# Optimization experiments

Hardware: AMD Instinct MI355X
Metric: run time of the kernel (lower is better)

## Reference

```python
import jax, jax.numpy as jnp
import numpy as np

N_NODES = 200000
D_FEAT = 128
B = 40000
DEG = 16
E = B * DEG
D_OUT = 256
N_CLASSES = 128


def setup_inputs() -> dict:
    key = jax.random.key(0)
    ks = jax.random.split(key, 8)
    inputs = jax.random.randint(ks[0], (B,), 0, N_NODES)
    neighbor_ids = jax.random.randint(ks[1], (E,), 0, N_NODES)
    segment_ids = jnp.repeat(jnp.arange(B, dtype=jnp.int64 if jax.config.jax_enable_x64 else jnp.int32), DEG)
    feat_data = jax.random.normal(ks[2], (N_NODES, D_FEAT), dtype=jnp.float32)
    W1 = jax.random.normal(ks[3], (D_OUT, 2 * D_FEAT), dtype=jnp.float32) * 0.05
    b1 = jax.random.normal(ks[4], (D_OUT,), dtype=jnp.float32) * 0.05
    W3 = jax.random.normal(ks[5], (N_CLASSES, D_OUT), dtype=jnp.float32) * 0.05
    b3 = jax.random.normal(ks[6], (N_CLASSES,), dtype=jnp.float32) * 0.05
    return {"inputs": inputs, "neighbor_ids": neighbor_ids, "segment_ids": segment_ids,
            "feat_data": feat_data, "W1": W1, "b1": b1, "W3": W3, "b3": b3}


def reference(inputs, neighbor_ids, segment_ids, feat_data, W1, b1, W3, b3):
    # Segment-mean over neighbor features (replaces Python per-node loop)
    neigh = feat_data[neighbor_ids]                               # [E, D]
    sums = jax.ops.segment_sum(neigh, segment_ids, num_segments=B)  # [B, D]
    cnt = jax.ops.segment_sum(jnp.ones((E,), jnp.float32), segment_ids, num_segments=B)
    means = sums / jnp.maximum(cnt, 1.0)[:, None]                 # [B, D]
    # Concat self + neighbor-mean, linear1
    emb = jnp.concatenate([feat_data[inputs], means], axis=1)     # [B, 2D]
    h = emb @ W1.T + b1                                           # [B, D_OUT]
    # ReLU -> linear3 -> L2 normalize (F.normalize, eps=1e-12)
    logits = jax.nn.relu(h) @ W3.T + b3                           # [B, n_classes]
    norm = jnp.linalg.norm(logits, axis=1, keepdims=True)
    return logits / jnp.maximum(norm, 1e-12)
```

## Files before the change

### kernel.cpp

```cpp
#include <hip/hip_runtime.h>
#include <stdint.h>

#define NNODES 200000
#define BNODES 40000
#define DEG    16
#define DFEAT  128
#define DOUT   256
#define NCLS   128
#define TILE   16

typedef __attribute__((ext_vector_type(8))) __bf16 bf16x8;
typedef __attribute__((ext_vector_type(4))) float  floatx4;

__device__ __forceinline__ uint32_t f2bf(float f) {
  uint32_t x = __float_as_uint(f);
  return ((x + 0x7fffu + ((x >> 16) & 1u)) >> 16) & 0xffffu;
}
__device__ __forceinline__ float bf2f(uint16_t u) {
  return __uint_as_float((uint32_t)u << 16);
}

__global__ __launch_bounds__(256) void cvt_weights(
    const float* __restrict__ W1, const float* __restrict__ W3,
    uint16_t* __restrict__ w1b, uint16_t* __restrict__ w3b) {
  int i = blockIdx.x * 256 + threadIdx.x;
  if (i < DOUT * 2 * DFEAT) w1b[i] = (uint16_t)f2bf(W1[i]);
  if (i < NCLS * DOUT)      w3b[i] = (uint16_t)f2bf(W3[i]);
}

__global__ __launch_bounds__(256) void cvt_feat(
    const float* __restrict__ feat, uint16_t* __restrict__ featb) {
  const size_t i = ((size_t)blockIdx.x * 256 + threadIdx.x) * 16;
  const float4 f0 = *(const float4*)(feat + i + 0);
  const float4 f1 = *(const float4*)(feat + i + 4);
  const float4 f2 = *(const float4*)(feat + i + 8);
  const float4 f3 = *(const float4*)(feat + i + 12);
  uint4 p0, p1;
  p0.x = f2bf(f0.x) | (f2bf(f0.y) << 16);
  p0.y = f2bf(f0.z) | (f2bf(f0.w) << 16);
  p0.z = f2bf(f1.x) | (f2bf(f1.y) << 16);
  p0.w = f2bf(f1.z) | (f2bf(f1.w) << 16);
  p1.x = f2bf(f2.x) | (f2bf(f2.y) << 16);
  p1.y = f2bf(f2.z) | (f2bf(f2.w) << 16);
  p1.z = f2bf(f3.x) | (f2bf(f3.y) << 16);
  p1.w = f2bf(f3.z) | (f2bf(f3.w) << 16);
  *(uint4*)(featb + i)     = p0;
  *(uint4*)(featb + i + 8) = p1;
}

template <bool BF16T>
__global__ __launch_bounds__(256, 8) void sage_fused(
    const int* __restrict__ inputs, const int* __restrict__ nbr,
    const float* __restrict__ feat, const uint16_t* __restrict__ featb,
    const uint16_t* __restrict__ w1b, const float* __restrict__ b1,
    const uint16_t* __restrict__ w3b, const float* __restrict__ b3,
    float* __restrict__ out) {
  __shared__ __align__(16) unsigned char smemA[TILE * 264 * 2];
  __shared__ __align__(16) uint16_t hL[TILE][264];
  uint16_t (*embL)[264] = (uint16_t (*)[264])smemA;
  float    (*lgL)[132]  = (float    (*)[132])smemA;

  const int tid  = threadIdx.x;
  const int w    = __builtin_amdgcn_readfirstlane(tid >> 6);
  const int lane = tid & 63;
  const int quad = lane >> 4;
  const int l16  = lane & 15;

  {
    const int nodeBase = blockIdx.x * TILE + w * 4;
    if constexpr (BF16T) {
      const uint16_t* fb = featb + lane * 2;
#pragma unroll
      for (int p = 0; p < 4; p += 2) {
        const int nA = nodeBase + p, nB = nodeBase + p + 1;
        const int* nbA = nbr + nA * DEG;
        const int* nbB = nbr + nB * DEG;
        const int sA = inputs[nA], sB = inputs[nB];
        ushort2 rA[16], rB[16];
#pragma unroll
        for (int j = 0; j < 16; ++j)
          rA[j] = *(const ushort2*)(fb + (size_t)nbA[j] * DFEAT);
        const ushort2 svA = *(const ushort2*)(fb + (size_t)sA * DFEAT);
#pragma unroll
        for (int j = 0; j < 16; ++j)
          rB[j] = *(const ushort2*)(fb + (size_t)nbB[j] * DFEAT);
        const ushort2 svB = *(const ushort2*)(fb + (size_t)sB * DFEAT);
        {
          const float sx = (((bf2f(rA[0].x) + bf2f(rA[1].x)) + (bf2f(rA[2].x) + bf2f(rA[3].x)))
                          + ((bf2f(rA[4].x) + bf2f(rA[5].x)) + (bf2f(rA[6].x) + bf2f(rA[7].x))))
                         + (((bf2f(rA[8].x) + bf2f(rA[9].x)) + (bf2f(rA[10].x) + bf2f(rA[11].x)))
                          + ((bf2f(rA[12].x) + bf2f(rA[13].x)) + (bf2f(rA[14].x) + bf2f(rA[15].x))));
          const float sy = (((bf2f(rA[0].y) + bf2f(rA[1].y)) + (bf2f(rA[2].y) + bf2f(rA[3].y)))
                          + ((bf2f(rA[4].y) + bf2f(rA[5].y)) + (bf2f(rA[6].y) + bf2f(rA[7].y))))
                         + (((bf2f(rA[8].y) + bf2f(rA[9].y)) + (bf2f(rA[10].y) + bf2f(rA[11].y)))
                          + ((bf2f(rA[12].y) + bf2f(rA[13].y)) + (bf2f(rA[14].y) + bf2f(rA[15].y))));
          const int row = w * 4 + p;
          *(uint32_t*)&embL[row][lane * 2]         = (uint32_t)svA.x | ((uint32_t)svA.y << 16);
          *(uint32_t*)&embL[row][DFEAT + lane * 2] = f2bf(sx * 0.0625f) | (f2bf(sy * 0.0625f) << 16);
        }
        {
          const float sx = (((bf2f(rB[0].x) + bf2f(rB[1].x)) + (bf2f(rB[2].x) + bf2f(rB[3].x)))
                          + ((bf2f(rB[4].x) + bf2f(rB[5].x)) + (bf2f(rB[6].x) + bf2f(rB[7].x))))
                         + (((bf2f(rB[8].x) + bf2f(rB[9].x)) + (bf2f(rB[10].x) + bf2f(rB[11].x)))
                          + ((bf2f(rB[12].x) + bf2f(rB[13].x)) + (bf2f(rB[14].x) + bf2f(rB[15].x))));
          const float sy = (((bf2f(rB[0].y) + bf2f(rB[1].y)) + (bf2f(rB[2].y) + bf2f(rB[3].y)))
                          + ((bf2f(rB[4].y) + bf2f(rB[5].y)) + (bf2f(rB[6].y) + bf2f(rB[7].y))))
                         + (((bf2f(rB[8].y) + bf2f(rB[9].y)) + (bf2f(rB[10].y) + bf2f(rB[11].y)))
                          + ((bf2f(rB[12].y) + bf2f(rB[13].y)) + (bf2f(rB[14].y) + bf2f(rB[15].y))));
          const int row = w * 4 + p + 1;
          *(uint32_t*)&embL[row][lane * 2]         = (uint32_t)svB.x | ((uint32_t)svB.y << 16);
          *(uint32_t*)&embL[row][DFEAT + lane * 2] = f2bf(sx * 0.0625f) | (f2bf(sy * 0.0625f) << 16);
        }
      }
    } else {
      const float* fb = feat + lane * 2;
#pragma unroll
      for (int p = 0; p < 4; ++p) {
        const int node = nodeBase + p;
        const int* nb  = nbr + node * DEG;
        const int self = inputs[node];
        float2 r[16];
#pragma unroll
        for (int j = 0; j < 16; ++j)
          r[j] = *(const float2*)(fb + (size_t)nb[j] * DFEAT);
        const float2 sv = *(const float2*)(fb + (size_t)self * DFEAT);
        const float sx = (((r[0].x + r[1].x) + (r[2].x + r[3].x)) + ((r[4].x + r[5].x) + (r[6].x + r[7].x)))
                       + (((r[8].x + r[9].x) + (r[10].x + r[11].x)) + ((r[12].x + r[13].x) + (r[14].x + r[15].x)));
        const float sy = (((r[0].y + r[1].y) + (r[2].y + r[3].y)) + ((r[4].y + r[5].y) + (r[6].y + r[7].y)))
                       + (((r[8].y + r[9].y) + (r[10].y + r[11].y)) + ((r[12].y + r[13].y) + (r[14].y + r[15].y)));
        const int row = w * 4 + p;
        *(uint32_t*)&embL[row][lane * 2]         = f2bf(sv.x) | (f2bf(sv.y) << 16);
        *(uint32_t*)&embL[row][DFEAT + lane * 2] = f2bf(sx * 0.0625f) | (f2bf(sy * 0.0625f) << 16);
      }
    }
  }
  __syncthreads();

  const int kq = quad * 8;

  {
    floatx4 acc[4];
#pragma unroll
    for (int ot = 0; ot < 4; ++ot) {
      floatx4 z = {0.f, 0.f, 0.f, 0.f};
      acc[ot] = z;
    }
#pragma unroll
    for (int kt = 0; kt < 8; ++kt) {
      const int k0 = kt * 32 + kq;
      const bf16x8 a = *(const bf16x8*)&embL[l16][k0];
#pragma unroll
      for (int ot = 0; ot < 4; ++ot) {
        const int o = w * 64 + ot * 16 + l16;
        const bf16x8 b = *(const bf16x8*)(w1b + o * 256 + k0);
        acc[ot] = __builtin_amdgcn_mfma_f32_16x16x32_bf16(a, b, acc[ot], 0, 0, 0);
      }
    }
#pragma unroll
    for (int ot = 0; ot < 4; ++ot) {
      const int o = w * 64 + ot * 16 + l16;
      const float bias = b1[o];
#pragma unroll
      for (int r = 0; r < 4; ++r) {
        float v = acc[ot][r] + bias;
        v = fmaxf(v, 0.f);
        hL[quad * 4 + r][o] = (uint16_t)f2bf(v);
      }
    }
  }
  __syncthreads();

  {
    floatx4 acc2[2];
#pragma unroll
    for (int ct = 0; ct < 2; ++ct) {
      floatx4 z = {0.f, 0.f, 0.f, 0.f};
      acc2[ct] = z;
    }
#pragma unroll
    for (int kt = 0; kt < 8; ++kt) {
      const int k0 = kt * 32 + kq;
      const bf16x8 a = *(const bf16x8*)&hL[l16][k0];
#pragma unroll
      for (int ct = 0; ct < 2; ++ct) {
        const int c = w * 32 + ct * 16 + l16;
        const bf16x8 b = *(const bf16x8*)(w3b + c * 256 + k0);
        acc2[ct] = __builtin_amdgcn_mfma_f32_16x16x32_bf16(a, b, acc2[ct], 0, 0, 0);
      }
    }
#pragma unroll
    for (int ct = 0; ct < 2; ++ct) {
      const int c = w * 32 + ct * 16 + l16;
      const float bias = b3[c];
#pragma unroll
      for (int r = 0; r < 4; ++r)
        lgL[quad * 4 + r][c] = acc2[ct][r] + bias;
    }
  }
  __syncthreads();

  {
    const int nr  = tid >> 4;
    const int sub = tid & 15;
    const float* lrow = &lgL[nr][sub * 8];
    float4 v0 = *(const float4*)(lrow + 0);
    float4 v1 = *(const float4*)(lrow + 4);
    float ss = v0.x * v0.x + v0.y * v0.y + v0.z * v0.z + v0.w * v0.w
             + v1.x * v1.x + v1.y * v1.y + v1.z * v1.z + v1.w * v1.w;
    ss += __shfl_xor(ss, 1);
    ss += __shfl_xor(ss, 2);
    ss += __shfl_xor(ss, 4);
    ss += __shfl_xor(ss, 8);
    const float scale = 1.f / fmaxf(sqrtf(ss), 1e-12f);
    v0.x *= scale; v0.y *= scale; v0.z *= scale; v0.w *= scale;
    v1.x *= scale; v1.y *= scale; v1.z *= scale; v1.w *= scale;
    float* op = out + ((size_t)(blockIdx.x * TILE + nr)) * NCLS + sub * 8;
    *(float4*)(op + 0) = v0;
    *(float4*)(op + 4) = v1;
  }
}

extern "C" void kernel_launch(void* const* d_in, const int* in_sizes, int n_in,
                              void* d_out, int out_size, void* d_ws, size_t ws_size,
                              hipStream_t stream) {
  const int*   inputs = (const int*)d_in[0];
  const int*   nbr    = (const int*)d_in[1];
  const float* feat   = (const float*)d_in[3];
  const float* W1     = (const float*)d_in[4];
  const float* b1     = (const float*)d_in[5];
  const float* W3     = (const float*)d_in[6];
  const float* b3     = (const float*)d_in[7];

  uint16_t* w1b   = (uint16_t*)d_ws;
  uint16_t* w3b   = w1b + DOUT * 2 * DFEAT;
  uint16_t* featb = w3b + NCLS * DOUT;

  const size_t need = ((size_t)(DOUT * 2 * DFEAT + NCLS * DOUT)
                     + (size_t)NNODES * DFEAT) * sizeof(uint16_t);

  cvt_weights<<<(DOUT * 2 * DFEAT) / 256, 256, 0, stream>>>(W1, W3, w1b, w3b);
  if (ws_size >= need) {
    cvt_feat<<<(NNODES * DFEAT) / (256 * 16), 256, 0, stream>>>(feat, featb);
    sage_fused<true><<<BNODES / TILE, 256, 0, stream>>>(
        inputs, nbr, feat, featb, w1b, b1, w3b, b3, (float*)d_out);
  } else {
    sage_fused<false><<<BNODES / TILE, 256, 0, stream>>>(
        inputs, nbr, feat, nullptr, w1b, b1, w3b, b3, (float*)d_out);
  }
}
```

Before: 246.5 us.

## Store gathered neighbor features as FP8 and fuse conversion kernels

Converts the feature table to a custom FP8 (e4m3-like) encoding instead of bf16, halving the bytes written during conversion and read during the neighbor gather. The gather is restructured so each lane loads 8 bytes from one of four neighbors and partial sums are combined with cross-lane shuffles. Self features are now read directly from the fp32 table. The weight and feature conversion kernels are merged into one launch, and the occupancy hint drops from 8 to 6 waves. The cost is reduced precision of the neighbor mean, which risks accuracy tolerance.

```diff
diff --git a/kernel.cpp b/kernel.cpp
--- a/kernel.cpp
+++ b/kernel.cpp
@@ -9,6 +9,8 @@
 #define NCLS   128
 #define TILE   16
 
+#define FEAT_CVT_BLOCKS 6250
+
 typedef __attribute__((ext_vector_type(8))) __bf16 bf16x8;
 typedef __attribute__((ext_vector_type(4))) float  floatx4;
 
@@ -16,8 +18,23 @@
   uint32_t x = __float_as_uint(f);
   return ((x + 0x7fffu + ((x >> 16) & 1u)) >> 16) & 0xffffu;
 }
-__device__ __forceinline__ float bf2f(uint16_t u) {
-  return __uint_as_float((uint32_t)u << 16);
+
+__device__ __forceinline__ uint32_t f2fp8(float f) {
+  uint32_t u = __float_as_uint(f);
+  uint32_t s = (u >> 24) & 0x80u;
+  uint32_t a = u & 0x7fffffffu;
+  if (a >= 0x43E80000u) return s | 0x7Eu;
+  if (a < 0x3C800000u) {
+    uint32_t q = (uint32_t)rintf(__uint_as_float(a) * 512.0f);
+    return s | q;
+  }
+  uint32_t r = a + 0x7FFFFu + ((a >> 20) & 1u);
+  return s | ((r >> 20) - (120u << 3));
+}
+
+__device__ __forceinline__ float fp82f(uint32_t b) {
+  uint32_t x = ((b & 0x80u) << 24) | ((b & 0x7Fu) << 20);
+  return __uint_as_float(x) * __uint_as_float(0x7B800000u);
 }
 
 __global__ __launch_bounds__(256) void cvt_weights(
@@ -28,30 +45,34 @@
   if (i < NCLS * DOUT)      w3b[i] = (uint16_t)f2bf(W3[i]);
 }
 
-__global__ __launch_bounds__(256) void cvt_feat(
-    const float* __restrict__ feat, uint16_t* __restrict__ featb) {
-  const size_t i = ((size_t)blockIdx.x * 256 + threadIdx.x) * 16;
-  const float4 f0 = *(const float4*)(feat + i + 0);
-  const float4 f1 = *(const float4*)(feat + i + 4);
-  const float4 f2 = *(const float4*)(feat + i + 8);
-  const float4 f3 = *(const float4*)(feat + i + 12);
-  uint4 p0, p1;
-  p0.x = f2bf(f0.x) | (f2bf(f0.y) << 16);
-  p0.y = f2bf(f0.z) | (f2bf(f0.w) << 16);
-  p0.z = f2bf(f1.x) | (f2bf(f1.y) << 16);
-  p0.w = f2bf(f1.z) | (f2bf(f1.w) << 16);
-  p1.x = f2bf(f2.x) | (f2bf(f2.y) << 16);
-  p1.y = f2bf(f2.z) | (f2bf(f2.w) << 16);
-  p1.z = f2bf(f3.x) | (f2bf(f3.y) << 16);
-  p1.w = f2bf(f3.z) | (f2bf(f3.w) << 16);
-  *(uint4*)(featb + i)     = p0;
-  *(uint4*)(featb + i + 8) = p1;
-}
-
-template <bool BF16T>
-__global__ __launch_bounds__(256, 8) void sage_fused(
+__global__ __launch_bounds__(256) void cvt_all(
+    const float* __restrict__ feat, const float* __restrict__ W1,
+    const float* __restrict__ W3, uint8_t* __restrict__ featb8,
+    uint16_t* __restrict__ w1b, uint16_t* __restrict__ w3b) {
+  const int b = blockIdx.x;
+  if (b < FEAT_CVT_BLOCKS) {
+    const size_t i = ((size_t)b * 256 + threadIdx.x) * 16;
+    const float4 f0 = *(const float4*)(feat + i + 0);
+    const float4 f1 = *(const float4*)(feat + i + 4);
+    const float4 f2 = *(const float4*)(feat + i + 8);
+    const float4 f3 = *(const float4*)(feat + i + 12);
+    uint4 p;
+    p.x = f2fp8(f0.x) | (f2fp8(f0.y) << 8) | (f2fp8(f0.z) << 16) | (f2fp8(f0.w) << 24);
+    p.y = f2fp8(f1.x) | (f2fp8(f1.y) << 8) | (f2fp8(f1.z) << 16) | (f2fp8(f1.w) << 24);
+    p.z = f2fp8(f2.x) | (f2fp8(f2.y) << 8) | (f2fp8(f2.z) << 16) | (f2fp8(f2.w) << 24);
+    p.w = f2fp8(f3.x) | (f2fp8(f3.y) << 8) | (f2fp8(f3.z) << 16) | (f2fp8(f3.w) << 24);
+    *(uint4*)(featb8 + i) = p;
+  } else {
+    const int i = (b - FEAT_CVT_BLOCKS) * 256 + threadIdx.x;
+    if (i < DOUT * 2 * DFEAT) w1b[i] = (uint16_t)f2bf(W1[i]);
+    if (i < NCLS * DOUT)      w3b[i] = (uint16_t)f2bf(W3[i]);
+  }
+}
+
+template <bool FP8T>
+__global__ __launch_bounds__(256, 6) void sage_fused(
     const int* __restrict__ inputs, const int* __restrict__ nbr,
-    const float* __restrict__ feat, const uint16_t* __restrict__ featb,
+    const float* __restrict__ feat, const uint8_t* __restrict__ featb8,
     const uint16_t* __restrict__ w1b, const float* __restrict__ b1,
     const uint16_t* __restrict__ w3b, const float* __restrict__ b3,
     float* __restrict__ out) {
@@ -68,48 +89,63 @@
 
   {
     const int nodeBase = blockIdx.x * TILE + w * 4;
-    if constexpr (BF16T) {
-      const uint16_t* fb = featb + lane * 2;
+    if constexpr (FP8T) {
+      const uint8_t* fb = featb8 + (lane & 15) * 8;
 #pragma unroll
       for (int p = 0; p < 4; p += 2) {
         const int nA = nodeBase + p, nB = nodeBase + p + 1;
         const int* nbA = nbr + nA * DEG;
         const int* nbB = nbr + nB * DEG;
         const int sA = inputs[nA], sB = inputs[nB];
-        ushort2 rA[16], rB[16];
-#pragma unroll
-        for (int j = 0; j < 16; ++j)
-          rA[j] = *(const ushort2*)(fb + (size_t)nbA[j] * DFEAT);
-        const ushort2 svA = *(const ushort2*)(fb + (size_t)sA * DFEAT);
-#pragma unroll
-        for (int j = 0; j < 16; ++j)
-          rB[j] = *(const ushort2*)(fb + (size_t)nbB[j] * DFEAT);
-        const ushort2 svB = *(const ushort2*)(fb + (size_t)sB * DFEAT);
-        {
-          const float sx = (((bf2f(rA[0].x) + bf2f(rA[1].x)) + (bf2f(rA[2].x) + bf2f(rA[3].x)))
-                          + ((bf2f(rA[4].x) + bf2f(rA[5].x)) + (bf2f(rA[6].x) + bf2f(rA[7].x))))
-                         + (((bf2f(rA[8].x) + bf2f(rA[9].x)) + (bf2f(rA[10].x) + bf2f(rA[11].x)))
-                          + ((bf2f(rA[12].x) + bf2f(rA[13].x)) + (bf2f(rA[14].x) + bf2f(rA[15].x))));
-          const float sy = (((bf2f(rA[0].y) + bf2f(rA[1].y)) + (bf2f(rA[2].y) + bf2f(rA[3].y)))
-                          + ((bf2f(rA[4].y) + bf2f(rA[5].y)) + (bf2f(rA[6].y) + bf2f(rA[7].y))))
-                         + (((bf2f(rA[8].y) + bf2f(rA[9].y)) + (bf2f(rA[10].y) + bf2f(rA[11].y)))
-                          + ((bf2f(rA[12].y) + bf2f(rA[13].y)) + (bf2f(rA[14].y) + bf2f(rA[15].y))));
-          const int row = w * 4 + p;
-          *(uint32_t*)&embL[row][lane * 2]         = (uint32_t)svA.x | ((uint32_t)svA.y << 16);
-          *(uint32_t*)&embL[row][DFEAT + lane * 2] = f2bf(sx * 0.0625f) | (f2bf(sy * 0.0625f) << 16);
+        uint2 gA[4], gB[4];
+#pragma unroll
+        for (int k = 0; k < 4; ++k) {
+          const int i0 = nbA[4 * k + 0], i1 = nbA[4 * k + 1];
+          const int i2 = nbA[4 * k + 2], i3 = nbA[4 * k + 3];
+          const int lo  = (lane & 16) ? i1 : i0;
+          const int hi  = (lane & 16) ? i3 : i2;
+          const int rid = (lane & 32) ? hi : lo;
+          gA[k] = *(const uint2*)(fb + (size_t)rid * DFEAT);
         }
-        {
-          const float sx = (((bf2f(rB[0].x) + bf2f(rB[1].x)) + (bf2f(rB[2].x) + bf2f(rB[3].x)))
-                          + ((bf2f(rB[4].x) + bf2f(rB[5].x)) + (bf2f(rB[6].x) + bf2f(rB[7].x))))
-                         + (((bf2f(rB[8].x) + bf2f(rB[9].x)) + (bf2f(rB[10].x) + bf2f(rB[11].x)))
-                          + ((bf2f(rB[12].x) + bf2f(rB[13].x)) + (bf2f(rB[14].x) + bf2f(rB[15].x))));
-          const float sy = (((bf2f(rB[0].y) + bf2f(rB[1].y)) + (bf2f(rB[2].y) + bf2f(rB[3].y)))
-                          + ((bf2f(rB[4].y) + bf2f(rB[5].y)) + (bf2f(rB[6].y) + bf2f(rB[7].y))))
-                         + (((bf2f(rB[8].y) + bf2f(rB[9].y)) + (bf2f(rB[10].y) + bf2f(rB[11].y)))
-                          + ((bf2f(rB[12].y) + bf2f(rB[13].y)) + (bf2f(rB[14].y) + bf2f(rB[15].y))));
-          const int row = w * 4 + p + 1;
-          *(uint32_t*)&embL[row][lane * 2]         = (uint32_t)svB.x | ((uint32_t)svB.y << 16);
-          *(uint32_t*)&embL[row][DFEAT + lane * 2] = f2bf(sx * 0.0625f) | (f2bf(sy * 0.0625f) << 16);
+        const float2 svA = *(const float2*)(feat + (size_t)sA * DFEAT + lane * 2);
+#pragma unroll
+        for (int k = 0; k < 4; ++k) {
+          const int i0 = nbB[4 * k + 0], i1 = nbB[4 * k + 1];
+          const int i2 = nbB[4 * k + 2], i3 = nbB[4 * k + 3];
+          const int lo  = (lane & 16) ? i1 : i0;
+          const int hi  = (lane & 16) ? i3 : i2;
+          const int rid = (lane & 32) ? hi : lo;
+          gB[k] = *(const uint2*)(fb + (size_t)rid * DFEAT);
+        }
+        const float2 svB = *(const float2*)(feat + (size_t)sB * DFEAT + lane * 2);
+#pragma unroll
+        for (int nn = 0; nn < 2; ++nn) {
+          const uint2* g = nn ? gB : gA;
+          const float2 sv = nn ? svB : svA;
+          const int row = w * 4 + p + nn;
+          float acc[8] = {0.f, 0.f, 0.f, 0.f, 0.f, 0.f, 0.f, 0.f};
+#pragma unroll
+          for (int k = 0; k < 4; ++k) {
+            const uint32_t lo = g[k].x, hi = g[k].y;
+#pragma unroll
+            for (int j = 0; j < 4; ++j) {
+              acc[j]     += fp82f((lo >> (8 * j)) & 0xffu);
+              acc[4 + j] += fp82f((hi >> (8 * j)) & 0xffu);
+            }
+          }
+#pragma unroll
+          for (int j = 0; j < 8; ++j) {
+            acc[j] += __shfl_xor(acc[j], 16);
+            acc[j] += __shfl_xor(acc[j], 32);
+          }
+          uint4 mp;
+          mp.x = f2bf(acc[0] * 0.0625f) | (f2bf(acc[1] * 0.0625f) << 16);
+          mp.y = f2bf(acc[2] * 0.0625f) | (f2bf(acc[3] * 0.0625f) << 16);
+          mp.z = f2bf(acc[4] * 0.0625f) | (f2bf(acc[5] * 0.0625f) << 16);
+          mp.w = f2bf(acc[6] * 0.0625f) | (f2bf(acc[7] * 0.0625f) << 16);
+          *(uint32_t*)&embL[row][lane * 2] = f2bf(sv.x) | (f2bf(sv.y) << 16);
+          if (lane < 16)
+            *(uint4*)&embL[row][DFEAT + lane * 8] = mp;
         }
       }
     } else {
@@ -231,19 +267,20 @@
   const float* W3     = (const float*)d_in[6];
   const float* b3     = (const float*)d_in[7];
 
-  uint16_t* w1b   = (uint16_t*)d_ws;
-  uint16_t* w3b   = w1b + DOUT * 2 * DFEAT;
-  uint16_t* featb = w3b + NCLS * DOUT;
-
-  const size_t need = ((size_t)(DOUT * 2 * DFEAT + NCLS * DOUT)
-                     + (size_t)NNODES * DFEAT) * sizeof(uint16_t);
-
-  cvt_weights<<<(DOUT * 2 * DFEAT) / 256, 256, 0, stream>>>(W1, W3, w1b, w3b);
+  uint16_t* w1b    = (uint16_t*)d_ws;
+  uint16_t* w3b    = w1b + DOUT * 2 * DFEAT;
+  uint8_t*  featb8 = (uint8_t*)(w3b + NCLS * DOUT);
+
+  const size_t need = (size_t)(DOUT * 2 * DFEAT + NCLS * DOUT) * sizeof(uint16_t)
+                    + (size_t)NNODES * DFEAT;
+
   if (ws_size >= need) {
-    cvt_feat<<<(NNODES * DFEAT) / (256 * 16), 256, 0, stream>>>(feat, featb);
+    cvt_all<<<FEAT_CVT_BLOCKS + (DOUT * 2 * DFEAT) / 256, 256, 0, stream>>>(
+        feat, W1, W3, featb8, w1b, w3b);
     sage_fused<true><<<BNODES / TILE, 256, 0, stream>>>(
-        inputs, nbr, feat, featb, w1b, b1, w3b, b3, (float*)d_out);
+        inputs, nbr, feat, featb8, w1b, b1, w3b, b3, (float*)d_out);
   } else {
+    cvt_weights<<<(DOUT * 2 * DFEAT) / 256, 256, 0, stream>>>(W1, W3, w1b, w3b);
     sage_fused<false><<<BNODES / TILE, 256, 0, stream>>>(
         inputs, nbr, feat, nullptr, w1b, b1, w3b, b3, (float*)d_out);
   }
```

Measured after the change: 238.6 us. 1.03x faster.

## Drop feature bf16 pre-conversion; split into fp32 gather kernel and MLP kernel

Applied to the files above, without the earlier changes.

Removes the full-table fp32-to-bf16 conversion pass over all 200k feature rows and instead gathers fp32 features directly in a dedicated gather/mean kernel that writes a bf16 embedding buffer. A separate MLP kernel loads that buffer and runs the two MFMA layers plus normalization. This avoids reading and writing the whole feature table every call, but the gather now reads fp32 rows (twice the bytes) and adds an intermediate global round-trip and an extra launch.

```diff
diff --git a/kernel.cpp b/kernel.cpp
--- a/kernel.cpp
+++ b/kernel.cpp
@@ -16,9 +16,6 @@
   uint32_t x = __float_as_uint(f);
   return ((x + 0x7fffu + ((x >> 16) & 1u)) >> 16) & 0xffffu;
 }
-__device__ __forceinline__ float bf2f(uint16_t u) {
-  return __uint_as_float((uint32_t)u << 16);
-}
 
 __global__ __launch_bounds__(256) void cvt_weights(
     const float* __restrict__ W1, const float* __restrict__ W3,
@@ -28,30 +25,35 @@
   if (i < NCLS * DOUT)      w3b[i] = (uint16_t)f2bf(W3[i]);
 }
 
-__global__ __launch_bounds__(256) void cvt_feat(
-    const float* __restrict__ feat, uint16_t* __restrict__ featb) {
-  const size_t i = ((size_t)blockIdx.x * 256 + threadIdx.x) * 16;
-  const float4 f0 = *(const float4*)(feat + i + 0);
-  const float4 f1 = *(const float4*)(feat + i + 4);
-  const float4 f2 = *(const float4*)(feat + i + 8);
-  const float4 f3 = *(const float4*)(feat + i + 12);
-  uint4 p0, p1;
-  p0.x = f2bf(f0.x) | (f2bf(f0.y) << 16);
-  p0.y = f2bf(f0.z) | (f2bf(f0.w) << 16);
-  p0.z = f2bf(f1.x) | (f2bf(f1.y) << 16);
-  p0.w = f2bf(f1.z) | (f2bf(f1.w) << 16);
-  p1.x = f2bf(f2.x) | (f2bf(f2.y) << 16);
-  p1.y = f2bf(f2.z) | (f2bf(f2.w) << 16);
-  p1.z = f2bf(f3.x) | (f2bf(f3.y) << 16);
-  p1.w = f2bf(f3.z) | (f2bf(f3.w) << 16);
-  *(uint4*)(featb + i)     = p0;
-  *(uint4*)(featb + i + 8) = p1;
-}
-
-template <bool BF16T>
-__global__ __launch_bounds__(256, 8) void sage_fused(
+__global__ __launch_bounds__(256, 8) void gather_mean(
     const int* __restrict__ inputs, const int* __restrict__ nbr,
-    const float* __restrict__ feat, const uint16_t* __restrict__ featb,
+    const float* __restrict__ feat, uint16_t* __restrict__ emb) {
+  const int w    = __builtin_amdgcn_readfirstlane(threadIdx.x >> 6);
+  const int lane = threadIdx.x & 63;
+  const int waveId = blockIdx.x * 4 + w;
+  const float* fb = feat + lane * 2;
+#pragma unroll
+  for (int p = 0; p < 4; ++p) {
+    const int node = waveId * 4 + p;
+    const int* nb  = nbr + node * DEG;
+    const int self = inputs[node];
+    float2 r[16];
+#pragma unroll
+    for (int j = 0; j < 16; ++j)
+      r[j] = *(const float2*)(fb + (size_t)nb[j] * DFEAT);
+    const float2 sv = *(const float2*)(fb + (size_t)self * DFEAT);
+    const float sx = (((r[0].x + r[1].x) + (r[2].x + r[3].x)) + ((r[4].x + r[5].x) + (r[6].x + r[7].x)))
+                   + (((r[8].x + r[9].x) + (r[10].x + r[11].x)) + ((r[12].x + r[13].x) + (r[14].x + r[15].x)));
+    const float sy = (((r[0].y + r[1].y) + (r[2].y + r[3].y)) + ((r[4].y + r[5].y) + (r[6].y + r[7].y)))
+                   + (((r[8].y + r[9].y) + (r[10].y + r[11].y)) + ((r[12].y + r[13].y) + (r[14].y + r[15].y)));
+    uint16_t* er = emb + (size_t)node * (2 * DFEAT);
+    *(uint32_t*)(er + lane * 2)         = f2bf(sv.x) | (f2bf(sv.y) << 16);
+    *(uint32_t*)(er + DFEAT + lane * 2) = f2bf(sx * 0.0625f) | (f2bf(sy * 0.0625f) << 16);
+  }
+}
+
+__global__ __launch_bounds__(256, 8) void sage_mlp(
+    const uint16_t* __restrict__ emb,
     const uint16_t* __restrict__ w1b, const float* __restrict__ b1,
     const uint16_t* __restrict__ w3b, const float* __restrict__ b3,
     float* __restrict__ out) {
@@ -67,72 +69,13 @@
   const int l16  = lane & 15;
 
   {
-    const int nodeBase = blockIdx.x * TILE + w * 4;
-    if constexpr (BF16T) {
-      const uint16_t* fb = featb + lane * 2;
-#pragma unroll
-      for (int p = 0; p < 4; p += 2) {
-        const int nA = nodeBase + p, nB = nodeBase + p + 1;
-        const int* nbA = nbr + nA * DEG;
-        const int* nbB = nbr + nB * DEG;
-        const int sA = inputs[nA], sB = inputs[nB];
-        ushort2 rA[16], rB[16];
-#pragma unroll
-        for (int j = 0; j < 16; ++j)
-          rA[j] = *(const ushort2*)(fb + (size_t)nbA[j] * DFEAT);
-        const ushort2 svA = *(const ushort2*)(fb + (size_t)sA * DFEAT);
-#pragma unroll
-        for (int j = 0; j < 16; ++j)
-          rB[j] = *(const ushort2*)(fb + (size_t)nbB[j] * DFEAT);
-        const ushort2 svB = *(const ushort2*)(fb + (size_t)sB * DFEAT);
-        {
-          const float sx = (((bf2f(rA[0].x) + bf2f(rA[1].x)) + (bf2f(rA[2].x) + bf2f(rA[3].x)))
-                          + ((bf2f(rA[4].x) + bf2f(rA[5].x)) + (bf2f(rA[6].x) + bf2f(rA[7].x))))
-                         + (((bf2f(rA[8].x) + bf2f(rA[9].x)) + (bf2f(rA[10].x) + bf2f(rA[11].x)))
-                          + ((bf2f(rA[12].x) + bf2f(rA[13].x)) + (bf2f(rA[14].x) + bf2f(rA[15].x))));
-          const float sy = (((bf2f(rA[0].y) + bf2f(rA[1].y)) + (bf2f(rA[2].y) + bf2f(rA[3].y)))
-                          + ((bf2f(rA[4].y) + bf2f(rA[5].y)) + (bf2f(rA[6].y) + bf2f(rA[7].y))))
-                         + (((bf2f(rA[8].y) + bf2f(rA[9].y)) + (bf2f(rA[10].y) + bf2f(rA[11].y)))
-                          + ((bf2f(rA[12].y) + bf2f(rA[13].y)) + (bf2f(rA[14].y) + bf2f(rA[15].y))));
-          const int row = w * 4 + p;
-          *(uint32_t*)&embL[row][lane * 2]         = (uint32_t)svA.x | ((uint32_t)svA.y << 16);
-          *(uint32_t*)&embL[row][DFEAT + lane * 2] = f2bf(sx * 0.0625f) | (f2bf(sy * 0.0625f) << 16);
-        }
-        {
-          const float sx = (((bf2f(rB[0].x) + bf2f(rB[1].x)) + (bf2f(rB[2].x) + bf2f(rB[3].x)))
-                          + ((bf2f(rB[4].x) + bf2f(rB[5].x)) + (bf2f(rB[6].x) + bf2f(rB[7].x))))
-                         + (((bf2f(rB[8].x) + bf2f(rB[9].x)) + (bf2f(rB[10].x) + bf2f(rB[11].x)))
-                          + ((bf2f(rB[12].x) + bf2f(rB[13].x)) + (bf2f(rB[14].x) + bf2f(rB[15].x))));
-          const float sy = (((bf2f(rB[0].y) + bf2f(rB[1].y)) + (bf2f(rB[2].y) + bf2f(rB[3].y)))
-                          + ((bf2f(rB[4].y) + bf2f(rB[5].y)) + (bf2f(rB[6].y) + bf2f(rB[7].y))))
-                         + (((bf2f(rB[8].y) + bf2f(rB[9].y)) + (bf2f(rB[10].y) + bf2f(rB[11].y)))
-                          + ((bf2f(rB[12].y) + bf2f(rB[13].y)) + (bf2f(rB[14].y) + bf2f(rB[15].y))));
-          const int row = w * 4 + p + 1;
-          *(uint32_t*)&embL[row][lane * 2]         = (uint32_t)svB.x | ((uint32_t)svB.y << 16);
-          *(uint32_t*)&embL[row][DFEAT + lane * 2] = f2bf(sx * 0.0625f) | (f2bf(sy * 0.0625f) << 16);
-        }
-      }
-    } else {
-      const float* fb = feat + lane * 2;
-#pragma unroll
-      for (int p = 0; p < 4; ++p) {
-        const int node = nodeBase + p;
-        const int* nb  = nbr + node * DEG;
-        const int self = inputs[node];
-        float2 r[16];
-#pragma unroll
-        for (int j = 0; j < 16; ++j)
-          r[j] = *(const float2*)(fb + (size_t)nb[j] * DFEAT);
-        const float2 sv = *(const float2*)(fb + (size_t)self * DFEAT);
-        const float sx = (((r[0].x + r[1].x) + (r[2].x + r[3].x)) + ((r[4].x + r[5].x) + (r[6].x + r[7].x)))
-                       + (((r[8].x + r[9].x) + (r[10].x + r[11].x)) + ((r[12].x + r[13].x) + (r[14].x + r[15].x)));
-        const float sy = (((r[0].y + r[1].y) + (r[2].y + r[3].y)) + ((r[4].y + r[5].y) + (r[6].y + r[7].y)))
-                       + (((r[8].y + r[9].y) + (r[10].y + r[11].y)) + ((r[12].y + r[13].y) + (r[14].y + r[15].y)));
-        const int row = w * 4 + p;
-        *(uint32_t*)&embL[row][lane * 2]         = f2bf(sv.x) | (f2bf(sv.y) << 16);
-        *(uint32_t*)&embL[row][DFEAT + lane * 2] = f2bf(sx * 0.0625f) | (f2bf(sy * 0.0625f) << 16);
-      }
-    }
+    const int r = tid >> 4;
+    const int c = tid & 15;
+    const uint16_t* er = emb + ((size_t)(blockIdx.x * TILE + r)) * (2 * DFEAT) + c * 16;
+    const uint4 v0 = *(const uint4*)(er + 0);
+    const uint4 v1 = *(const uint4*)(er + 8);
+    *(uint4*)&embL[r][c * 16 + 0] = v0;
+    *(uint4*)&embL[r][c * 16 + 8] = v1;
   }
   __syncthreads();
 
@@ -220,6 +163,128 @@
   }
 }
 
+__global__ __launch_bounds__(256, 8) void sage_fused_fb(
+    const int* __restrict__ inputs, const int* __restrict__ nbr,
+    const float* __restrict__ feat,
+    const uint16_t* __restrict__ w1b, const float* __restrict__ b1,
+    const uint16_t* __restrict__ w3b, const float* __restrict__ b3,
+    float* __restrict__ out) {
+  __shared__ __align__(16) unsigned char smemA[TILE * 264 * 2];
+  __shared__ __align__(16) uint16_t hL[TILE][264];
+  uint16_t (*embL)[264] = (uint16_t (*)[264])smemA;
+  float    (*lgL)[132]  = (float    (*)[132])smemA;
+
+  const int tid  = threadIdx.x;
+  const int w    = __builtin_amdgcn_readfirstlane(tid >> 6);
+  const int lane = tid & 63;
+  const int quad = lane >> 4;
+  const int l16  = lane & 15;
+
+  {
+    const int nodeBase = blockIdx.x * TILE + w * 4;
+    const float* fb = feat + lane * 2;
+#pragma unroll
+    for (int p = 0; p < 4; ++p) {
+      const int node = nodeBase + p;
+      const int* nb  = nbr + node * DEG;
+      const int self = inputs[node];
+      float2 r[16];
+#pragma unroll
+      for (int j = 0; j < 16; ++j)
+        r[j] = *(const float2*)(fb + (size_t)nb[j] * DFEAT);
+      const float2 sv = *(const float2*)(fb + (size_t)self * DFEAT);
+      const float sx = (((r[0].x + r[1].x) + (r[2].x + r[3].x)) + ((r[4].x + r[5].x) + (r[6].x + r[7].x)))
+                     + (((r[8].x + r[9].x) + (r[10].x + r[11].x)) + ((r[12].x + r[13].x) + (r[14].x + r[15].x)));
+      const float sy = (((r[0].y + r[1].y) + (r[2].y + r[3].y)) + ((r[4].y + r[5].y) + (r[6].y + r[7].y)))
+                     + (((r[8].y + r[9].y) + (r[10].y + r[11].y)) + ((r[12].y + r[13].y) + (r[14].y + r[15].y)));
+      const int row = w * 4 + p;
+      *(uint32_t*)&embL[row][lane * 2]         = f2bf(sv.x) | (f2bf(sv.y) << 16);
+      *(uint32_t*)&embL[row][DFEAT + lane * 2] = f2bf(sx * 0.0625f) | (f2bf(sy * 0.0625f) << 16);
+    }
+  }
+  __syncthreads();
+
+  const int kq = quad * 8;
+  {
+    floatx4 acc[4];
+#pragma unroll
+    for (int ot = 0; ot < 4; ++ot) {
+      floatx4 z = {0.f, 0.f, 0.f, 0.f};
+      acc[ot] = z;
+    }
+#pragma unroll
+    for (int kt = 0; kt < 8; ++kt) {
+      const int k0 = kt * 32 + kq;
+      const bf16x8 a = *(const bf16x8*)&embL[l16][k0];
+#pragma unroll
+      for (int ot = 0; ot < 4; ++ot) {
+        const int o = w * 64 + ot * 16 + l16;
+        const bf16x8 b = *(const bf16x8*)(w1b + o * 256 + k0);
+        acc[ot] = __builtin_amdgcn_mfma_f32_16x16x32_bf16(a, b, acc[ot], 0, 0, 0);
+      }
+    }
+#pragma unroll
+    for (int ot = 0; ot < 4; ++ot) {
+      const int o = w * 64 + ot * 16 + l16;
+      const float bias = b1[o];
+#pragma unroll
+      for (int r = 0; r < 4; ++r) {
+        float v = acc[ot][r] + bias;
+        v = fmaxf(v, 0.f);
+        hL[quad * 4 + r][o] = (uint16_t)f2bf(v);
+      }
+    }
+  }
+  __syncthreads();
+  {
+    floatx4 acc2[2];
+#pragma unroll
+    for (int ct = 0; ct < 2; ++ct) {
+      floatx4 z = {0.f, 0.f, 0.f, 0.f};
+      acc2[ct] = z;
+    }
+#pragma unroll
+    for (int kt = 0; kt < 8; ++kt) {
+      const int k0 = kt * 32 + kq;
+      const bf16x8 a = *(const bf16x8*)&hL[l16][k0];
+#pragma unroll
+      for (int ct = 0; ct < 2; ++ct) {
+        const int c = w * 32 + ct * 16 + l16;
+        const bf16x8 b = *(const bf16x8*)(w3b + c * 256 + k0);
+        acc2[ct] = __builtin_amdgcn_mfma_f32_16x16x32_bf16(a, b, acc2[ct], 0, 0, 0);
+      }
+    }
+#pragma unroll
+    for (int ct = 0; ct < 2; ++ct) {
+      const int c = w * 32 + ct * 16 + l16;
+      const float bias = b3[c];
+#pragma unroll
+      for (int r = 0; r < 4; ++r)
+        lgL[quad * 4 + r][c] = acc2[ct][r] + bias;
+    }
+  }
+  __syncthreads();
+  {
+    const int nr  = tid >> 4;
+    const int sub = tid & 15;
+    const float* lrow = &lgL[nr][sub * 8];
+    float4 v0 = *(const float4*)(lrow + 0);
+    float4 v1 = *(const float4*)(lrow + 4);
+    float ss = v0.x * v0.x + v0.y * v0.y + v0.z * v0.z + v0.w * v0.w
+             + v1.x * v1.x + v1.y * v1.y + v1.z * v1.z + v1.w * v1.w;
+    ss += __shfl_xor(ss, 1);
+    ss += __shfl_xor(ss, 2);
+    ss += __shfl_xor(ss, 4);
+    ss += __shfl_xor(ss, 8);
+    const float scale = 1.f / fmaxf(sqrtf(ss), 1e-12f);
+    v0.x *= scale; v0.y *= scale; v0.z *= scale; v0.w *= scale;
+    v1.x *= scale; v1.y *= scale; v1.z *= scale; v1.w *= scale;
+    float* op = out + ((size_t)(blockIdx.x * TILE + nr)) * NCLS + sub * 8;
+    *(float4*)(op + 0) = v0;
+    *(float4*)(op + 4) = v1;
+  }
+}
+
 extern "C" void kernel_launch(void* const* d_in, const int* in_sizes, int n_in,
                               void* d_out, int out_size, void* d_ws, size_t ws_size,
                               hipStream_t stream) {
@@ -231,20 +296,20 @@
   const float* W3     = (const float*)d_in[6];
   const float* b3     = (const float*)d_in[7];
 
-  uint16_t* w1b   = (uint16_t*)d_ws;
-  uint16_t* w3b   = w1b + DOUT * 2 * DFEAT;
-  uint16_t* featb = w3b + NCLS * DOUT;
+  uint16_t* w1b = (uint16_t*)d_ws;
+  uint16_t* w3b = w1b + DOUT * 2 * DFEAT;
+  uint16_t* emb = w3b + NCLS * DOUT;
 
   const size_t need = ((size_t)(DOUT * 2 * DFEAT + NCLS * DOUT)
-                     + (size_t)NNODES * DFEAT) * sizeof(uint16_t);
+                     + (size_t)BNODES * 2 * DFEAT) * sizeof(uint16_t);
 
   cvt_weights<<<(DOUT * 2 * DFEAT) / 256, 256, 0, stream>>>(W1, W3, w1b, w3b);
   if (ws_size >= need) {
-    cvt_feat<<<(NNODES * DFEAT) / (256 * 16), 256, 0, stream>>>(feat, featb);
-    sage_fused<true><<<BNODES / TILE, 256, 0, stream>>>(
-        inputs, nbr, feat, featb, w1b, b1, w3b, b3, (float*)d_out);
+    gather_mean<<<BNODES / TILE, 256, 0, stream>>>(inputs, nbr, feat, emb);
+    sage_mlp<<<BNODES / TILE, 256, 0, stream>>>(emb, w1b, b1, w3b, b3,
+                                                (float*)d_out);
   } else {
-    sage_fused<false><<<BNODES / TILE, 256, 0, stream>>>(
-        inputs, nbr, feat, nullptr, w1b, b1, w3b, b3, (float*)d_out);
-  }
-}
+    sage_fused_fb<<<BNODES / TILE, 256, 0, stream>>>(inputs, nbr, feat, w1b, b1,
+                                                     w3b, b3, (float*)d_out);
+  }
+}
```

Measured after the change: 256.1 us. +3.9%, slower.
